# Optimization experiments

Hardware: AMD Instinct MI355X
Metric: run time of the kernel (lower is better)

Reference implementation:

```python
import jax, jax.numpy as jnp
import numpy as np

IN_F = 512
OUT_F = 512
ALPHA = 0.2  # LeakyReLU negative slope
# dropout p=0.1 is a no-op at inference (training=False), so omitted


def setup_inputs() -> dict:
    key = jax.random.key(0)
    k1, k2, k3 = jax.random.split(key, 3)
    B, N = 16, 1024
    x = jax.random.normal(k1, (B, N, IN_F), dtype=jnp.float32)
    # xavier_uniform with gain=1.414
    limW = 1.414 * np.sqrt(6.0 / (IN_F + OUT_F))
    W = jax.random.uniform(k2, (IN_F, OUT_F), minval=-limW, maxval=limW, dtype=jnp.float32)
    lima = 1.414 * np.sqrt(6.0 / (2 * OUT_F + 1))
    a = jax.random.uniform(k3, (2 * OUT_F, 1), minval=-lima, maxval=lima, dtype=jnp.float32)
    beta = jnp.ones((1,), dtype=jnp.float32)
    return {"x": x, "W": W, "a": a, "beta": beta}


def reference(x, W, a, beta):
    # h: [B, N, F]
    h = jnp.matmul(x, W)
    # Split attention vector: e_ij = leakyrelu(h_i . a1 + h_j . a2)
    a1 = a[:OUT_F, 0]   # [F]
    a2 = a[OUT_F:, 0]   # [F]
    s1 = jnp.einsum('bnf,f->bn', h, a1)  # [B, N]
    s2 = jnp.einsum('bnf,f->bn', h, a2)  # [B, N]
    e = s1[:, :, None] + s2[:, None, :]  # [B, N, N]
    e = jnp.where(e > 0, e, ALPHA * e)   # LeakyReLU
    attention = jax.nn.softmax(e, axis=2)
    h_prime = jnp.einsum('bnm,bmf->bnf', attention, h)
    out = jax.nn.elu(h_prime + beta * h)
    return out
```

## Files before the change

kernel.cpp:

```cpp
#include <hip/hip_runtime.h>

using u16 = unsigned short;
using u32 = unsigned int;
using u64 = unsigned long long;

#define ALPHA 0.2f
#define LOG2E 1.4426950408889634f

typedef __bf16 bf16x8 __attribute__((ext_vector_type(8)));
typedef float f32x4 __attribute__((ext_vector_type(4)));
typedef float f32x16 __attribute__((ext_vector_type(16)));

__device__ __forceinline__ u16 f2bf(float f) {
  u32 u = __builtin_bit_cast(u32, f);
  u += 0x7FFFu + ((u >> 16) & 1u);
  return (u16)(u >> 16);
}
__device__ __forceinline__ float bf2f(u16 h) {
  u32 u = ((u32)h) << 16;
  return __builtin_bit_cast(float, u);
}
__device__ __forceinline__ void gload_lds16(const void* g, void* l) {
  __builtin_amdgcn_global_load_lds((__attribute__((address_space(1))) void*)g,
                                   (__attribute__((address_space(3))) void*)l,
                                   16, 0, 0);
}

__global__ __launch_bounds__(256) void k_cast_wT(const float* __restrict__ W, u16* __restrict__ wbt) {
  int idx = blockIdx.x * 256 + threadIdx.x;
  int k = idx >> 9, n = idx & 511;
  wbt[n * 512 + k] = f2bf(W[idx]);
}

__global__ __launch_bounds__(256, 2) void k_gemm1(const float* __restrict__ x, const u16* __restrict__ wbt,
                                                  const float* __restrict__ a,
                                                  u16* __restrict__ hbf,
                                                  float* __restrict__ s1p, float* __restrict__ s2p) {
  __shared__ __attribute__((aligned(16))) char lds[73728];
  __shared__ __attribute__((aligned(16))) float a_l[256];

  const int t = threadIdx.x;
  const int lane = t & 63;
  const int w = t >> 6;
  const int l31 = lane & 31, lhi = lane >> 5;
  const int rb = w >> 1, cg = w & 1;
  const int g = blockIdx.x;
  const int cb = (g >> 3) & 3;
  const int tile_m = (g & 7) | ((g >> 5) << 3);
  const int row0 = tile_m * 128;
  const int col0 = cb * 128;

  a_l[t] = (t < 128) ? a[col0 + t] : a[512 + col0 + (t - 128)];

  f32x16 acc[2][2];
#pragma unroll
  for (int i = 0; i < 2; ++i)
#pragma unroll
    for (int j = 0; j < 2; ++j)
#pragma unroll
      for (int r = 0; r < 16; ++r) acc[i][j][r] = 0.f;

#define STAGE_G1(kt, Ab, Bb)                                                              \
  {                                                                                       \
    const int k0_ = (kt) * 32;                                                            \
    _Pragma("unroll")                                                                     \
    for (int i = 0; i < 4; ++i) {                                                         \
      int G = i * 256 + t;                                                                \
      int row = G >> 3, ks = G & 7;                                                       \
      gload_lds16(x + (size_t)(row0 + row) * 512 + k0_ + ((ks ^ (row & 7)) * 4),          \
                  (Ab) + (size_t)(i * 256 + w * 64) * 16);                                \
    }                                                                                     \
    _Pragma("unroll")                                                                     \
    for (int i = 0; i < 2; ++i) {                                                         \
      int G = i * 256 + t;                                                                \
      int col = G >> 2, ks = G & 3;                                                       \
      gload_lds16(wbt + (size_t)(col0 + col) * 512 + k0_ + ((ks ^ ((col >> 1) & 3)) * 8), \
                  (Bb) + (size_t)(i * 256 + w * 64) * 16);                                \
    }                                                                                     \
  }

#define COMPUTE_G1(Ab, Bb)                                                                         \
  {                                                                                                \
    _Pragma("unroll")                                                                              \
    for (int ks = 0; ks < 2; ++ks) {                                                               \
      bf16x8 af[2];                                                                                \
      _Pragma("unroll")                                                                            \
      for (int sub = 0; sub < 2; ++sub) {                                                          \
        const int arow = rb * 64 + sub * 32 + l31;                                                 \
        const int kg = ks * 4 + lhi * 2;                                                           \
        f32x4 fa0 = *reinterpret_cast<const f32x4*>((Ab) + (size_t)(arow * 8 + (kg ^ (arow & 7))) * 16); \
        f32x4 fa1 = *reinterpret_cast<const f32x4*>((Ab) + (size_t)(arow * 8 + ((kg + 1) ^ (arow & 7))) * 16); \
        _Pragma("unroll")                                                                          \
        for (int jj = 0; jj < 4; ++jj) {                                                           \
          af[sub][jj] = (__bf16)fa0[jj];                                                           \
          af[sub][jj + 4] = (__bf16)fa1[jj];                                                       \
        }                                                                                          \
      }                                                                                            \
      bf16x8 bfr[2];                                                                               \
      _Pragma("unroll")                                                                            \
      for (int bt = 0; bt < 2; ++bt) {                                                             \
        const int bcol = cg * 64 + bt * 32 + l31;                                                  \
        const int kslot = (ks * 2 + lhi) ^ ((bcol >> 1) & 3);                                      \
        bfr[bt] = *reinterpret_cast<const bf16x8*>((Bb) + (size_t)(bcol * 4 + kslot) * 16);        \
      }                                                                                            \
      _Pragma("unroll")                                                                            \
      for (int sub = 0; sub < 2; ++sub)                                                            \
        _Pragma("unroll")                                                                          \
        for (int bt = 0; bt < 2; ++bt)                                                             \
          acc[sub][bt] = __builtin_amdgcn_mfma_f32_32x32x16_bf16(af[sub], bfr[bt], acc[sub][bt], 0, 0, 0); \
    }                                                                                              \
  }

  char* Ac = lds;             char* Bc = lds + 49152;
  char* An = lds + 16384;     char* Bn = lds + 57344;
  char* As = lds + 32768;     char* Bs = lds + 65536;

  STAGE_G1(0, Ac, Bc);
  STAGE_G1(1, An, Bn);
  __builtin_amdgcn_sched_barrier(0);
  asm volatile("s_waitcnt vmcnt(6) lgkmcnt(0)" ::: "memory");
  __builtin_amdgcn_s_barrier();
  __builtin_amdgcn_sched_barrier(0);

#pragma unroll 1
  for (int kt = 0; kt < 14; ++kt) {
    STAGE_G1(kt + 2, As, Bs);
    COMPUTE_G1(Ac, Bc);
    __builtin_amdgcn_sched_barrier(0);
    asm volatile("s_waitcnt vmcnt(6)" ::: "memory");
    __builtin_amdgcn_s_barrier();
    __builtin_amdgcn_sched_barrier(0);
    char* ta = Ac; Ac = An; An = As; As = ta;
    char* tb = Bc; Bc = Bn; Bn = Bs; Bs = tb;
  }
  COMPUTE_G1(Ac, Bc);
  __builtin_amdgcn_sched_barrier(0);
  asm volatile("s_waitcnt vmcnt(0)" ::: "memory");
  __builtin_amdgcn_s_barrier();
  __builtin_amdgcn_sched_barrier(0);
  COMPUTE_G1(An, Bn);
#undef STAGE_G1
#undef COMPUTE_G1

  __syncthreads();

  u16* lT = (u16*)lds;
#pragma unroll
  for (int sub = 0; sub < 2; ++sub)
#pragma unroll
    for (int bt = 0; bt < 2; ++bt) {
      const int col = cg * 64 + bt * 32 + l31;
#pragma unroll
      for (int r = 0; r < 16; ++r) {
        int row = rb * 64 + sub * 32 + (r & 3) + 8 * (r >> 2) + 4 * lhi;
        lT[row * 136 + col] = f2bf(acc[sub][bt][r]);
      }
    }
  __syncthreads();

#pragma unroll
  for (int i = 0; i < 8; ++i) {
    int G = i * 256 + t;
    int row = G >> 4, gg = G & 15;
    uint4 v = *reinterpret_cast<const uint4*>(&lT[row * 136 + gg * 8]);
    *reinterpret_cast<uint4*>(&hbf[(size_t)(row0 + row) * 512 + col0 + gg * 8]) = v;
  }
  {
    const int r2 = t >> 1, half = t & 1;
    float d1 = 0.f, d2 = 0.f;
#pragma unroll
    for (int i = 0; i < 8; ++i) {
      uint4 v = *reinterpret_cast<const uint4*>(&lT[r2 * 136 + half * 64 + i * 8]);
      u32 wds[4] = {v.x, v.y, v.z, v.w};
#pragma unroll
      for (int jj = 0; jj < 8; ++jj) {
        float h = bf2f((u16)(wds[jj >> 1] >> ((jj & 1) * 16)));
        d1 += h * a_l[half * 64 + i * 8 + jj];
        d2 += h * a_l[128 + half * 64 + i * 8 + jj];
      }
    }
    d1 += __shfl_xor(d1, 1);
    d2 += __shfl_xor(d2, 1);
    if (half == 0) {
      s1p[cb * 16384 + row0 + r2] = d1;
      s2p[cb * 16384 + row0 + r2] = d2;
    }
  }
}

__global__ __launch_bounds__(1024) void k_prep(const float* __restrict__ s1p, const float* __restrict__ s2p,
                                               float* __restrict__ e1s, float* __restrict__ e2s,
                                               u32* __restrict__ permM, u32* __restrict__ kng,
                                               float* __restrict__ c1ig, float* __restrict__ c2ig) {
  __shared__ u32 sk[1024];
  __shared__ float s2all[1024];
  __shared__ float s2sv[1024];
  __shared__ float arrA[1024];
  __shared__ float arrB[1024];
  __shared__ float wtA[16], wtB[16];
  const int b = blockIdx.x;
  const int t = threadIdx.x;
  const int lane = t & 63, wid = t >> 6;
  const int id = b * 1024 + t;

  const float s1v = (s1p[id] + s1p[16384 + id] + s1p[32768 + id] + s1p[49152 + id]) * LOG2E;
  const float s2v = (s2p[id] + s2p[16384 + id] + s2p[32768 + id] + s2p[49152 + id]) * LOG2E;
  s2all[t] = s2v;

  u32 key;
  {
    u32 bits = __builtin_bit_cast(u32, s2v);
    u32 k2 = (bits & 0x80000000u) ? ~bits : (bits | 0x80000000u);
    key = (k2 & 0xFFFFFC00u) | (u32)t;
  }

#define SHFL_CE(size_, stride_)                                            \
  {                                                                        \
    u32 partner = (u32)__shfl_xor((int)key, (stride_));                    \
    bool dir = ((t & (size_)) == 0);                                       \
    bool keepMin = (dir == ((t & (stride_)) == 0));                        \
    key = keepMin ? (key < partner ? key : partner)                        \
                  : (key > partner ? key : partner);                       \
  }

#pragma unroll
  for (int size = 2; size <= 64; size <<= 1)
#pragma unroll
    for (int stride = size >> 1; stride > 0; stride >>= 1) SHFL_CE(size, stride);

#pragma unroll 1
  for (int size = 128; size <= 1024; size <<= 1) {
    sk[t] = key;
#pragma unroll 1
    for (int stride = size >> 1; stride >= 64; stride >>= 1) {
      __syncthreads();
      int ixj = t ^ stride;
      if (ixj > t) {
        u32 va = sk[t], vb = sk[ixj];
        bool asc = ((t & size) == 0);
        if ((va > vb) == asc) { sk[t] = vb; sk[ixj] = va; }
      }
    }
    __syncthreads();
    key = sk[t];
#pragma unroll
    for (int stride = 32; stride > 0; stride >>= 1) SHFL_CE(size, stride);
  }
#undef SHFL_CE

  const u32 idx = key & 1023u;
  const float sv = s2all[idx];
  s2sv[t] = sv;
  __syncthreads();

  const float E1 = exp2f(sv), E2 = exp2f(ALPHA * sv);
  e1s[b * 1024 + t] = E1;
  e2s[b * 1024 + t] = E2;
  permM[b * 1024 + t] = idx;

  float aA = E2;
  float aB = exp2f(s2sv[1023 - t]);
#pragma unroll
  for (int off = 1; off < 64; off <<= 1) {
    float uA = __shfl_up(aA, off);
    float uB = __shfl_up(aB, off);
    if (lane >= off) { aA += uA; aB += uB; }
  }
  if (lane == 63) { wtA[wid] = aA; wtB[wid] = aB; }
  __syncthreads();
  {
    float offA = 0.f, offB = 0.f;
#pragma unroll
    for (int i2 = 0; i2 < 16; ++i2) {
      float vA2 = wtA[i2], vB2 = wtB[i2];
      if (i2 < wid) { offA += vA2; offB += vB2; }
    }
    aA += offA;
    aB += offB;
  }
  arrA[t] = aA;
  arrB[t] = aB;
  __syncthreads();

  {
    const float thr = -s1v;
    int lo = 0, hi = 1024;
    while (lo < hi) { int mid = (lo + hi) >> 1; if (s2sv[mid] <= thr) lo = mid + 1; else hi = mid; }
    const int kn = lo;
    float se1suf = (kn == 1024) ? 0.f : arrB[1023 - kn];
    float se2pre = (kn == 0) ? 0.f : arrA[kn - 1];
    const float c1 = exp2f(s1v), c2 = exp2f(ALPHA * s1v);
    const float inv = 1.0f / (c1 * se1suf + c2 * se2pre);
    c1ig[id] = c1 * inv;
    c2ig[id] = c2 * inv;
    kng[id] = (u32)kn;
  }
}

__global__ __launch_bounds__(256, 4) void k_sweep2(const u16* __restrict__ hbf,
                                                   const float* __restrict__ e1s, const float* __restrict__ e2s,
                                                   const u32* __restrict__ permM, const u32* __restrict__ kng,
                                                   const float* __restrict__ c1ig, const float* __restrict__ c2ig,
                                                   const float* __restrict__ betag, float* __restrict__ out) {
  __shared__ u32 Cp[1060][8];
  __shared__ u16 kn_l[1024];
  __shared__ float segS1[32][8];
  __shared__ float segP2[32][8];

  const int t = threadIdx.x;
  const int B = blockIdx.x;
  const int b = (B & 7) * 2 + ((B >> 3) & 1);
  const int fc = B >> 4;

  const u16* hB = hbf + (size_t)b * 1024 * 512 + fc * 8;

#pragma unroll
  for (int q = 0; q < 4; ++q) {
    int i = q * 256 + t;
    kn_l[i] = (u16)kng[b * 1024 + i];
  }

  const int f = t & 7;
  const int seg = t >> 3;
  const int i0 = seg * 32;
  const int p0 = seg * 33;
  const u32* permB = permM + b * 1024 + i0;
  const float* e1B = e1s + b * 1024 + i0;
  const float* e2B = e2s + b * 1024 + i0;

  u32 hpk[16];
  float ss1 = 0.f, ss2 = 0.f;
#pragma unroll
  for (int c = 0; c < 32; c += 2) {
    u16 h0 = hB[(size_t)permB[c] * 512 + f];
    u16 h1 = hB[(size_t)permB[c + 1] * 512 + f];
    hpk[c >> 1] = (u32)h0 | ((u32)h1 << 16);
    ss1 = fmaf(e1B[c], bf2f(h0), ss1);
    ss1 = fmaf(e1B[c + 1], bf2f(h1), ss1);
    ss2 = fmaf(e2B[c], bf2f(h0), ss2);
    ss2 = fmaf(e2B[c + 1], bf2f(h1), ss2);
  }
  segS1[seg][f] = ss1;
  segP2[seg][f] = ss2;
  __syncthreads();

  float sufAfter = 0.f, preBefore = 0.f;
#pragma unroll
  for (int s7 = 0; s7 < 32; ++s7) {
    if (s7 > seg) sufAfter += segS1[s7][f];
    if (s7 < seg) preBefore += segP2[s7][f];
  }

  u32 c1p[16];
  {
    float run1 = sufAfter;
#pragma unroll
    for (int c = 31; c >= 0; --c) {
      u16 hv = (u16)(hpk[c >> 1] >> ((c & 1) * 16));
      run1 = fmaf(e1B[c], bf2f(hv), run1);
      if (c & 1) c1p[c >> 1] = (u32)f2bf(run1) << 16;
      else c1p[c >> 1] |= (u32)f2bf(run1);
    }
  }
  {
    float run2 = preBefore;
#pragma unroll
    for (int c = 0; c < 32; ++c) {
      u16 c1v = (u16)(c1p[c >> 1] >> ((c & 1) * 16));
      Cp[p0 + c][f] = (u32)c1v | ((u32)f2bf(run2) << 16);
      u16 hv = (u16)(hpk[c >> 1] >> ((c & 1) * 16));
      run2 = fmaf(e2B[c], bf2f(hv), run2);
    }
    if (seg == 31) Cp[1056][f] = (u32)f2bf(run2) << 16;
  }
  __syncthreads();

  const float beta = betag[0];
  const int nn = (t >> 3) & 7;
  const int wv = t >> 6;
  const float* c1B = c1ig + b * 1024;
  const float* c2B = c2ig + b * 1024;
#pragma unroll 4
  for (int r = 0; r < 32; ++r) {
    const int n = r * 32 + wv * 8 + nn;
    const int kn = (int)kn_l[n];
    const u32 cp = Cp[kn + (kn >> 5)][f];
    const float A = bf2f((u16)(cp & 0xFFFFu));
    const float Bv = bf2f((u16)(cp >> 16));
    const float hvn = bf2f(hB[(size_t)n * 512 + f]);
    const float xv = c1B[n] * A + c2B[n] * Bv + beta * hvn;
    out[((size_t)b * 1024 + n) * 512 + fc * 8 + f] = xv > 0.f ? xv : __expf(xv) - 1.0f;
  }
}

extern "C" void kernel_launch(void* const* d_in, const int* in_sizes, int n_in,
                              void* d_out, int out_size, void* d_ws, size_t ws_size,
                              hipStream_t stream) {
  const float* x = (const float*)d_in[0];
  const float* W = (const float*)d_in[1];
  const float* a = (const float*)d_in[2];
  const float* beta = (const float*)d_in[3];
  float* out = (float*)d_out;

  char* ws = (char*)d_ws;
  u16* hbf = (u16*)ws;
  char* sm = ws + (16u << 20);
  float* e1s = (float*)(sm);
  float* e2s = (float*)(sm + (64u << 10));
  u32* permM = (u32*)(sm + (128u << 10));
  u32* kng = (u32*)(sm + (192u << 10));
  float* c1i = (float*)(sm + (256u << 10));
  float* c2i = (float*)(sm + (320u << 10));
  float* s1p = (float*)(sm + (512u << 10));
  float* s2p = (float*)(sm + (768u << 10));
  u16* wbt = (u16*)(sm + (1024u << 10));

  k_cast_wT<<<1024, 256, 0, stream>>>(W, wbt);
  k_gemm1<<<512, 256, 0, stream>>>(x, wbt, a, hbf, s1p, s2p);
  k_prep<<<16, 1024, 0, stream>>>(s1p, s2p, e1s, e2s, permM, kng, c1i, c2i);
  k_sweep2<<<1024, 256, 0, stream>>>(hbf, e1s, e2s, permM, kng, c1i, c2i, beta, out);
}
```

Before: 60.15 us.

## Load GEMM1 B operand directly into registers and shrink LDS for higher occupancy

The bf16 W^T tile is no longer staged through LDS. Each lane loads its B fragments straight from global memory into registers, double-buffered across k-steps, while the fp32 x tile still goes through the triple-buffered LDS pipeline. This cuts LDS use from 72KB to 48KB, so launch bounds can rise to 3 blocks per CU. The trade-off is more register pressure and uncoalesced, redundant global reads of W, since waves with the same column group reload the same data.

```diff
diff --git a/kernel.cpp b/kernel.cpp
--- a/kernel.cpp
+++ b/kernel.cpp
@@ -32,11 +32,11 @@
   wbt[n * 512 + k] = f2bf(W[idx]);
 }
 
-__global__ __launch_bounds__(256, 2) void k_gemm1(const float* __restrict__ x, const u16* __restrict__ wbt,
+__global__ __launch_bounds__(256, 3) void k_gemm1(const float* __restrict__ x, const u16* __restrict__ wbt,
                                                   const float* __restrict__ a,
                                                   u16* __restrict__ hbf,
                                                   float* __restrict__ s1p, float* __restrict__ s2p) {
-  __shared__ __attribute__((aligned(16))) char lds[73728];
+  __shared__ __attribute__((aligned(16))) char lds[49152];
   __shared__ __attribute__((aligned(16))) float a_l[256];
 
   const int t = threadIdx.x;
@@ -60,26 +60,31 @@
 #pragma unroll
       for (int r = 0; r < 16; ++r) acc[i][j][r] = 0.f;
 
-#define STAGE_G1(kt, Ab, Bb)                                                              \
-  {                                                                                       \
-    const int k0_ = (kt) * 32;                                                            \
-    _Pragma("unroll")                                                                     \
-    for (int i = 0; i < 4; ++i) {                                                         \
-      int G = i * 256 + t;                                                                \
-      int row = G >> 3, ks = G & 7;                                                       \
-      gload_lds16(x + (size_t)(row0 + row) * 512 + k0_ + ((ks ^ (row & 7)) * 4),          \
-                  (Ab) + (size_t)(i * 256 + w * 64) * 16);                                \
-    }                                                                                     \
-    _Pragma("unroll")                                                                     \
-    for (int i = 0; i < 2; ++i) {                                                         \
-      int G = i * 256 + t;                                                                \
-      int col = G >> 2, ks = G & 3;                                                       \
-      gload_lds16(wbt + (size_t)(col0 + col) * 512 + k0_ + ((ks ^ ((col >> 1) & 3)) * 8), \
-                  (Bb) + (size_t)(i * 256 + w * 64) * 16);                                \
-    }                                                                                     \
-  }
-
-#define COMPUTE_G1(Ab, Bb)                                                                         \
+  const u16* wB = wbt + (size_t)(col0 + cg * 64 + l31) * 512;
+
+#define STAGE_A(kt, Ab)                                                          \
+  {                                                                              \
+    const int k0_ = (kt) * 32;                                                   \
+    _Pragma("unroll")                                                            \
+    for (int i = 0; i < 4; ++i) {                                                \
+      int G = i * 256 + t;                                                       \
+      int row = G >> 3, ks = G & 7;                                              \
+      gload_lds16(x + (size_t)(row0 + row) * 512 + k0_ + ((ks ^ (row & 7)) * 4), \
+                  (Ab) + (size_t)(i * 256 + w * 64) * 16);                       \
+    }                                                                            \
+  }
+
+#define LOAD_B(dst, kt)                                                                     \
+  {                                                                                         \
+    _Pragma("unroll")                                                                       \
+    for (int ks = 0; ks < 2; ++ks)                                                          \
+      _Pragma("unroll")                                                                     \
+      for (int bt = 0; bt < 2; ++bt)                                                        \
+        dst[ks][bt] = *reinterpret_cast<const bf16x8*>(wB + (size_t)(bt * 32) * 512 +       \
+                                                       (kt) * 32 + ks * 16 + lhi * 8);      \
+  }
+
+#define COMPUTE_B(Ab, Br)                                                                          \
   {                                                                                                \
     _Pragma("unroll")                                                                              \
     for (int ks = 0; ks < 2; ++ks) {                                                               \
@@ -96,51 +101,57 @@
           af[sub][jj + 4] = (__bf16)fa1[jj];                                                       \
         }                                                                                          \
       }                                                                                            \
-      bf16x8 bfr[2];                                                                               \
-      _Pragma("unroll")                                                                            \
-      for (int bt = 0; bt < 2; ++bt) {                                                             \
-        const int bcol = cg * 64 + bt * 32 + l31;                                                  \
-        const int kslot = (ks * 2 + lhi) ^ ((bcol >> 1) & 3);                                      \
-        bfr[bt] = *reinterpret_cast<const bf16x8*>((Bb) + (size_t)(bcol * 4 + kslot) * 16);        \
-      }                                                                                            \
       _Pragma("unroll")                                                                            \
       for (int sub = 0; sub < 2; ++sub)                                                            \
         _Pragma("unroll")                                                                          \
         for (int bt = 0; bt < 2; ++bt)                                                             \
-          acc[sub][bt] = __builtin_amdgcn_mfma_f32_32x32x16_bf16(af[sub], bfr[bt], acc[sub][bt], 0, 0, 0); \
+          acc[sub][bt] = __builtin_amdgcn_mfma_f32_32x32x16_bf16(af[sub], (Br)[ks][bt], acc[sub][bt], 0, 0, 0); \
     }                                                                                              \
   }
 
-  char* Ac = lds;             char* Bc = lds + 49152;
-  char* An = lds + 16384;     char* Bn = lds + 57344;
-  char* As = lds + 32768;     char* Bs = lds + 65536;
-
-  STAGE_G1(0, Ac, Bc);
-  STAGE_G1(1, An, Bn);
+  char* Ac = lds;
+  char* An = lds + 16384;
+  char* As = lds + 32768;
+  bf16x8 B0[2][2], B1[2][2];
+
+  STAGE_A(0, Ac);
+  STAGE_A(1, An);
+  LOAD_B(B0, 0);
   __builtin_amdgcn_sched_barrier(0);
-  asm volatile("s_waitcnt vmcnt(6) lgkmcnt(0)" ::: "memory");
+  asm volatile("s_waitcnt vmcnt(8) lgkmcnt(0)" ::: "memory");
   __builtin_amdgcn_s_barrier();
   __builtin_amdgcn_sched_barrier(0);
 
 #pragma unroll 1
-  for (int kt = 0; kt < 14; ++kt) {
-    STAGE_G1(kt + 2, As, Bs);
-    COMPUTE_G1(Ac, Bc);
+  for (int kt = 0; kt < 14; kt += 2) {
+    STAGE_A(kt + 2, As);
+    LOAD_B(B1, kt + 1);
+    COMPUTE_B(Ac, B0);
     __builtin_amdgcn_sched_barrier(0);
-    asm volatile("s_waitcnt vmcnt(6)" ::: "memory");
+    asm volatile("s_waitcnt vmcnt(8)" ::: "memory");
     __builtin_amdgcn_s_barrier();
     __builtin_amdgcn_sched_barrier(0);
     char* ta = Ac; Ac = An; An = As; As = ta;
-    char* tb = Bc; Bc = Bn; Bn = Bs; Bs = tb;
-  }
-  COMPUTE_G1(Ac, Bc);
+
+    STAGE_A(kt + 3, As);
+    LOAD_B(B0, kt + 2);
+    COMPUTE_B(Ac, B1);
+    __builtin_amdgcn_sched_barrier(0);
+    asm volatile("s_waitcnt vmcnt(8)" ::: "memory");
+    __builtin_amdgcn_s_barrier();
+    __builtin_amdgcn_sched_barrier(0);
+    char* tb = Ac; Ac = An; An = As; As = tb;
+  }
+  LOAD_B(B1, 15);
+  COMPUTE_B(Ac, B0);
   __builtin_amdgcn_sched_barrier(0);
   asm volatile("s_waitcnt vmcnt(0)" ::: "memory");
   __builtin_amdgcn_s_barrier();
   __builtin_amdgcn_sched_barrier(0);
-  COMPUTE_G1(An, Bn);
-#undef STAGE_G1
-#undef COMPUTE_G1
+  COMPUTE_B(An, B1);
+#undef STAGE_A
+#undef LOAD_B
+#undef COMPUTE_B
 
   __syncthreads();
 
```

Result: slower. 67.82 us (+12.8%).
